# Optimization experiments

Measured on AMD Instinct MI355X. Metric: run time of the kernel, lower is better.

Reference implementation:

```python
import jax, jax.numpy as jnp
import numpy as np

B, IN, HID, OUT = 65536, 128, 256, 8


def setup_inputs() -> dict:
    key = jax.random.key(0)
    ks = jax.random.split(key, 9)
    def lin(kw, fan_in, fan_out):
        # torch nn.Linear default init: U(-1/sqrt(fan_in), 1/sqrt(fan_in))
        bound = 1.0 / np.sqrt(fan_in)
        kw1, kw2 = jax.random.split(kw)
        W = jax.random.uniform(kw1, (fan_out, fan_in), jnp.float32, -bound, bound)
        b = jax.random.uniform(kw2, (fan_out,), jnp.float32, -bound, bound)
        return W, b
    W1, b1 = lin(ks[0], 2 * IN, HID)
    W2, b2 = lin(ks[1], 2 * IN, HID)
    W3, b3 = lin(ks[2], HID + 3 * IN, HID)
    W4, b4 = lin(ks[3], HID, OUT)
    state = jax.random.normal(ks[4], (B, 3, IN), jnp.float32)
    return {"state": state, "W1": W1, "b1": b1, "W2": W2, "b2": b2,
            "W3": W3, "b3": b3, "W4": W4, "b4": b4}


def reference(state, W1, b1, W2, b2, W3, b3, W4, b4):
    # local_inputs = first 3 agents (state already [B,3,IN])
    local = state[:, :3]                              # [B,3,IN]
    agent = jnp.broadcast_to(local[:, :1], (local.shape[0], 2, local.shape[2]))
    neighbors = local[:, 1:3]                          # [B,2,IN]
    agents = jnp.concatenate([agent, neighbors], axis=-1)  # [B,2,2*IN]
    h_ij = jax.nn.relu(jnp.einsum('bnd,hd->bnh', agents, W1) + b1)  # [B,2,HID]
    e_ij = jax.nn.relu(jnp.einsum('bnd,hd->bnh', agents, W2) + b2)  # [B,2,HID]
    a_ij = jax.nn.softmax(e_ij, axis=1)                # softmax over neighbor dim
    h_i = jnp.sum(a_ij * h_ij, axis=1)                 # [B,HID]
    xxx = jnp.concatenate([h_i, local.reshape(local.shape[0], -1)], axis=-1)
    xxx = jax.nn.relu(xxx @ W3.T + b3)                 # [B,HID]
    return jnp.tanh(xxx @ W4.T + b4)                   # [B,OUT]
```

## Files before the change

### kernel.cpp

```cpp
#include <hip/hip_runtime.h>

typedef __bf16 bf16x8 __attribute__((ext_vector_type(8)));
typedef float  f32x4  __attribute__((ext_vector_type(4)));

__device__ __forceinline__ unsigned short f2bf(float f) {
  unsigned int u = __builtin_bit_cast(unsigned int, f);
  u = u + 0x7fffu + ((u >> 16) & 1u);
  return (unsigned short)(u >> 16);
}

#define O_W2 65536
#define O_W3 131072
#define O_W4 294912
#define N_PREP 299008

__global__ void prep_kernel(const float* __restrict__ W1, const float* __restrict__ W2,
                            const float* __restrict__ W3, const float* __restrict__ W4,
                            unsigned short* __restrict__ ws) {
  int id = blockIdx.x * 256 + threadIdx.x;
  if (id < O_W2) {
    ws[id] = f2bf(W1[id]);
  } else if (id < O_W3) {
    ws[id] = f2bf(W2[id - O_W2]);
  } else if (id < O_W4) {
    ws[id] = f2bf(W3[id - O_W3]);
  } else if (id < N_PREP) {
    int t = id - O_W4;
    ws[id] = (t < 2048) ? f2bf(W4[t]) : (unsigned short)0;
  }
}

#define XSTR 648
#define YSTR 264

__global__ __launch_bounds__(512, 2) void actor_kernel(
    const float* __restrict__ state,
    const float* __restrict__ b1, const float* __restrict__ b2,
    const float* __restrict__ b3, const float* __restrict__ b4,
    const unsigned short* __restrict__ wsb,
    float* __restrict__ out)
{
  __shared__ unsigned short xxx[64 * XSTR];
  __shared__ unsigned short ytl[64 * YSTR];

  const int tid  = threadIdx.x;
  const int w    = tid >> 6;
  const int lane = tid & 63;
  const int lr   = lane & 15;
  const int lg   = lane >> 4;
  const long b0  = (long)blockIdx.x * 64;

  {
    const float4* sp = (const float4*)(state + b0 * 384);
    #pragma unroll
    for (int t = 0; t < 12; ++t) {
      int f = tid + t * 512;
      float4 v = sp[f];
      int r   = f / 96;
      int rem = f - r * 96;
      int i   = rem >> 5;
      int k4  = (rem & 31) << 2;
      ushort4 u;
      u.x = f2bf(v.x); u.y = f2bf(v.y); u.z = f2bf(v.z); u.w = f2bf(v.w);
      *(ushort4*)&xxx[r * XSTR + 256 + i * 128 + k4] = u;
    }
  }
  __syncthreads();

  const int n0 = w * 32;

  #pragma unroll
  for (int sc = 0; sc < 2; ++sc) {
    const int ncol = n0 + sc * 16 + lr;
    f32x4 accH[8], accE[8];
    #pragma unroll
    for (int rt = 0; rt < 8; ++rt) {
      accH[rt] = (f32x4){0.f, 0.f, 0.f, 0.f};
      accE[rt] = (f32x4){0.f, 0.f, 0.f, 0.f};
    }
    const unsigned short* w1p = wsb + ncol * 256 + lg * 8;
    const unsigned short* w2p = wsb + O_W2 + ncol * 256 + lg * 8;

    bf16x8 bh = *(const bf16x8*)(w1p);
    bf16x8 be = *(const bf16x8*)(w2p);
    #pragma unroll
    for (int ks = 0; ks < 8; ++ks) {
      bf16x8 bhn, ben;
      if (ks < 7) {
        bhn = *(const bf16x8*)(w1p + (ks + 1) * 32);
        ben = *(const bf16x8*)(w2p + (ks + 1) * 32);
      }
      const int colo = (ks < 4) ? (256 + ks * 32 + lg * 8)
                                : (384 + (ks - 4) * 32 + lg * 8);
      #pragma unroll
      for (int rt = 0; rt < 8; ++rt) {
        const int m = rt * 16 + lr;
        const int addr = (m >> 1) * XSTR + colo + ((ks >= 4) ? ((m & 1) << 7) : 0);
        bf16x8 a = *(const bf16x8*)&xxx[addr];
        accH[rt] = __builtin_amdgcn_mfma_f32_16x16x32_bf16(a, bh, accH[rt], 0, 0, 0);
        accE[rt] = __builtin_amdgcn_mfma_f32_16x16x32_bf16(a, be, accE[rt], 0, 0, 0);
      }
      bh = bhn; be = ben;
    }

    const float b1v = b1[ncol];
    const float b2v = b2[ncol];
    #pragma unroll
    for (int rt = 0; rt < 8; ++rt) {
      const int r0 = rt * 8 + lg * 2;
      #pragma unroll
      for (int pr = 0; pr < 2; ++pr) {
        float h0 = fmaxf(accH[rt][2 * pr + 0] + b1v, 0.f);
        float h1 = fmaxf(accH[rt][2 * pr + 1] + b1v, 0.f);
        float e0 = fmaxf(accE[rt][2 * pr + 0] + b2v, 0.f);
        float e1 = fmaxf(accE[rt][2 * pr + 1] + b2v, 0.f);
        float a0 = 1.0f / (1.0f + __expf(e1 - e0));
        float hi = h1 + a0 * (h0 - h1);
        xxx[(r0 + pr) * XSTR + ncol] = f2bf(hi);
      }
    }
  }
  __syncthreads();

  {
    f32x4 acc3[4][2];
    #pragma unroll
    for (int rt = 0; rt < 4; ++rt) {
      acc3[rt][0] = (f32x4){0.f, 0.f, 0.f, 0.f};
      acc3[rt][1] = (f32x4){0.f, 0.f, 0.f, 0.f};
    }
    const unsigned short* w3pa = wsb + O_W3 + (n0 + lr) * 640 + lg * 8;
    const unsigned short* w3pb = wsb + O_W3 + (n0 + 16 + lr) * 640 + lg * 8;
    bf16x8 ba = *(const bf16x8*)(w3pa);
    bf16x8 bb = *(const bf16x8*)(w3pb);
    for (int ks = 0; ks < 20; ++ks) {
      bf16x8 ban, bbn;
      if (ks < 19) {
        ban = *(const bf16x8*)(w3pa + (ks + 1) * 32);
        bbn = *(const bf16x8*)(w3pb + (ks + 1) * 32);
      }
      #pragma unroll
      for (int rt = 0; rt < 4; ++rt) {
        bf16x8 a = *(const bf16x8*)&xxx[(rt * 16 + lr) * XSTR + ks * 32 + lg * 8];
        acc3[rt][0] = __builtin_amdgcn_mfma_f32_16x16x32_bf16(a, ba, acc3[rt][0], 0, 0, 0);
        acc3[rt][1] = __builtin_amdgcn_mfma_f32_16x16x32_bf16(a, bb, acc3[rt][1], 0, 0, 0);
      }
      ba = ban; bb = bbn;
    }
    const float b3a = b3[n0 + lr];
    const float b3b = b3[n0 + 16 + lr];
    #pragma unroll
    for (int rt = 0; rt < 4; ++rt) {
      #pragma unroll
      for (int reg = 0; reg < 4; ++reg) {
        int row = rt * 16 + lg * 4 + reg;
        float va = fmaxf(acc3[rt][0][reg] + b3a, 0.f);
        float vb = fmaxf(acc3[rt][1][reg] + b3b, 0.f);
        ytl[row * YSTR + n0 + lr]      = f2bf(va);
        ytl[row * YSTR + n0 + 16 + lr] = f2bf(vb);
      }
    }
  }
  __syncthreads();

  if (w < 4) {
    f32x4 acc4 = (f32x4){0.f, 0.f, 0.f, 0.f};
    const unsigned short* w4p = wsb + O_W4 + lr * 256 + lg * 8;
    #pragma unroll
    for (int ks = 0; ks < 8; ++ks) {
      bf16x8 a = *(const bf16x8*)&ytl[(w * 16 + lr) * YSTR + ks * 32 + lg * 8];
      bf16x8 b = *(const bf16x8*)(w4p + ks * 32);
      acc4 = __builtin_amdgcn_mfma_f32_16x16x32_bf16(a, b, acc4, 0, 0, 0);
    }
    if (lr < 8) {
      const float b4v = b4[lr];
      #pragma unroll
      for (int reg = 0; reg < 4; ++reg) {
        long row = b0 + w * 16 + lg * 4 + reg;
        out[row * 8 + lr] = tanhf(acc4[reg] + b4v);
      }
    }
  }
}

extern "C" void kernel_launch(void* const* d_in, const int* in_sizes, int n_in,
                              void* d_out, int out_size, void* d_ws, size_t ws_size,
                              hipStream_t stream) {
  const float* state = (const float*)d_in[0];
  const float* W1 = (const float*)d_in[1];
  const float* b1 = (const float*)d_in[2];
  const float* W2 = (const float*)d_in[3];
  const float* b2 = (const float*)d_in[4];
  const float* W3 = (const float*)d_in[5];
  const float* b3 = (const float*)d_in[6];
  const float* W4 = (const float*)d_in[7];
  const float* b4 = (const float*)d_in[8];

  unsigned short* wsb = (unsigned short*)d_ws;

  prep_kernel<<<(N_PREP + 255) / 256, 256, 0, stream>>>(W1, W2, W3, W4, wsb);
  actor_kernel<<<1024, 512, 0, stream>>>(state, b1, b2, b3, b4, wsb, (float*)d_out);
}
```

Before: 241.6 us.

## Split layer-1 GEMM by agent, persist blocks over 4 tiles with double-buffered state prefetch

```diff
diff --git a/kernel.cpp b/kernel.cpp
--- a/kernel.cpp
+++ b/kernel.cpp
@@ -30,8 +30,9 @@
   }
 }
 
-#define XSTR 648
-#define YSTR 264
+#define SB(r, c) ((r) * 384 + ((c) ^ (((r) & 7) << 3)))
+#define SH(r, c) ((r) * 256 + ((c) ^ (((r) & 7) << 3)))
+#define MFMA __builtin_amdgcn_mfma_f32_16x16x32_bf16
 
 __global__ __launch_bounds__(512, 2) void actor_kernel(
     const float* __restrict__ state,
@@ -40,146 +41,185 @@
     const unsigned short* __restrict__ wsb,
     float* __restrict__ out)
 {
-  __shared__ unsigned short xxx[64 * XSTR];
-  __shared__ unsigned short ytl[64 * YSTR];
+  __shared__ __align__(16) unsigned short sbuf[2][64 * 384];
+  __shared__ __align__(16) unsigned short hy[64 * 256];
 
   const int tid  = threadIdx.x;
   const int w    = tid >> 6;
   const int lane = tid & 63;
   const int lr   = lane & 15;
   const int lg   = lane >> 4;
-  const long b0  = (long)blockIdx.x * 64;
+  const long blk = blockIdx.x;
 
   {
-    const float4* sp = (const float4*)(state + b0 * 384);
+    const float4* sp = (const float4*)(state + blk * 256 * 384);
     #pragma unroll
-    for (int t = 0; t < 12; ++t) {
-      int f = tid + t * 512;
+    for (int i = 0; i < 12; ++i) {
+      int f = tid + i * 512;
       float4 v = sp[f];
-      int r   = f / 96;
-      int rem = f - r * 96;
-      int i   = rem >> 5;
-      int k4  = (rem & 31) << 2;
+      int r = f / 96, rem = f - r * 96;
       ushort4 u;
       u.x = f2bf(v.x); u.y = f2bf(v.y); u.z = f2bf(v.z); u.w = f2bf(v.w);
-      *(ushort4*)&xxx[r * XSTR + 256 + i * 128 + k4] = u;
+      *(ushort4*)&sbuf[0][SB(r, rem * 4)] = u;
     }
   }
   __syncthreads();
 
-  const int n0 = w * 32;
-
-  #pragma unroll
-  for (int sc = 0; sc < 2; ++sc) {
-    const int ncol = n0 + sc * 16 + lr;
-    f32x4 accH[8], accE[8];
-    #pragma unroll
-    for (int rt = 0; rt < 8; ++rt) {
-      accH[rt] = (f32x4){0.f, 0.f, 0.f, 0.f};
-      accE[rt] = (f32x4){0.f, 0.f, 0.f, 0.f};
-    }
-    const unsigned short* w1p = wsb + ncol * 256 + lg * 8;
-    const unsigned short* w2p = wsb + O_W2 + ncol * 256 + lg * 8;
-
-    bf16x8 bh = *(const bf16x8*)(w1p);
-    bf16x8 be = *(const bf16x8*)(w2p);
-    #pragma unroll
-    for (int ks = 0; ks < 8; ++ks) {
-      bf16x8 bhn, ben;
-      if (ks < 7) {
-        bhn = *(const bf16x8*)(w1p + (ks + 1) * 32);
-        ben = *(const bf16x8*)(w2p + (ks + 1) * 32);
-      }
-      const int colo = (ks < 4) ? (256 + ks * 32 + lg * 8)
-                                : (384 + (ks - 4) * 32 + lg * 8);
-      #pragma unroll
-      for (int rt = 0; rt < 8; ++rt) {
-        const int m = rt * 16 + lr;
-        const int addr = (m >> 1) * XSTR + colo + ((ks >= 4) ? ((m & 1) << 7) : 0);
-        bf16x8 a = *(const bf16x8*)&xxx[addr];
-        accH[rt] = __builtin_amdgcn_mfma_f32_16x16x32_bf16(a, bh, accH[rt], 0, 0, 0);
-        accE[rt] = __builtin_amdgcn_mfma_f32_16x16x32_bf16(a, be, accE[rt], 0, 0, 0);
-      }
-      bh = bhn; be = ben;
-    }
-
-    const float b1v = b1[ncol];
-    const float b2v = b2[ncol];
-    #pragma unroll
-    for (int rt = 0; rt < 8; ++rt) {
-      const int r0 = rt * 8 + lg * 2;
-      #pragma unroll
-      for (int pr = 0; pr < 2; ++pr) {
-        float h0 = fmaxf(accH[rt][2 * pr + 0] + b1v, 0.f);
-        float h1 = fmaxf(accH[rt][2 * pr + 1] + b1v, 0.f);
-        float e0 = fmaxf(accE[rt][2 * pr + 0] + b2v, 0.f);
-        float e1 = fmaxf(accE[rt][2 * pr + 1] + b2v, 0.f);
-        float a0 = 1.0f / (1.0f + __expf(e1 - e0));
-        float hi = h1 + a0 * (h0 - h1);
-        xxx[(r0 + pr) * XSTR + ncol] = f2bf(hi);
-      }
-    }
-  }
-  __syncthreads();
-
-  {
-    f32x4 acc3[4][2];
-    #pragma unroll
-    for (int rt = 0; rt < 4; ++rt) {
-      acc3[rt][0] = (f32x4){0.f, 0.f, 0.f, 0.f};
-      acc3[rt][1] = (f32x4){0.f, 0.f, 0.f, 0.f};
-    }
-    const unsigned short* w3pa = wsb + O_W3 + (n0 + lr) * 640 + lg * 8;
-    const unsigned short* w3pb = wsb + O_W3 + (n0 + 16 + lr) * 640 + lg * 8;
-    bf16x8 ba = *(const bf16x8*)(w3pa);
-    bf16x8 bb = *(const bf16x8*)(w3pb);
-    for (int ks = 0; ks < 20; ++ks) {
-      bf16x8 ban, bbn;
-      if (ks < 19) {
-        ban = *(const bf16x8*)(w3pa + (ks + 1) * 32);
-        bbn = *(const bf16x8*)(w3pb + (ks + 1) * 32);
-      }
-      #pragma unroll
-      for (int rt = 0; rt < 4; ++rt) {
-        bf16x8 a = *(const bf16x8*)&xxx[(rt * 16 + lr) * XSTR + ks * 32 + lg * 8];
-        acc3[rt][0] = __builtin_amdgcn_mfma_f32_16x16x32_bf16(a, ba, acc3[rt][0], 0, 0, 0);
-        acc3[rt][1] = __builtin_amdgcn_mfma_f32_16x16x32_bf16(a, bb, acc3[rt][1], 0, 0, 0);
-      }
-      ba = ban; bb = bbn;
-    }
-    const float b3a = b3[n0 + lr];
-    const float b3b = b3[n0 + 16 + lr];
-    #pragma unroll
-    for (int rt = 0; rt < 4; ++rt) {
-      #pragma unroll
-      for (int reg = 0; reg < 4; ++reg) {
-        int row = rt * 16 + lg * 4 + reg;
-        float va = fmaxf(acc3[rt][0][reg] + b3a, 0.f);
-        float vb = fmaxf(acc3[rt][1][reg] + b3b, 0.f);
-        ytl[row * YSTR + n0 + lr]      = f2bf(va);
-        ytl[row * YSTR + n0 + 16 + lr] = f2bf(vb);
-      }
-    }
-  }
-  __syncthreads();
-
-  if (w < 4) {
-    f32x4 acc4 = (f32x4){0.f, 0.f, 0.f, 0.f};
-    const unsigned short* w4p = wsb + O_W4 + lr * 256 + lg * 8;
-    #pragma unroll
-    for (int ks = 0; ks < 8; ++ks) {
-      bf16x8 a = *(const bf16x8*)&ytl[(w * 16 + lr) * YSTR + ks * 32 + lg * 8];
-      bf16x8 b = *(const bf16x8*)(w4p + ks * 32);
-      acc4 = __builtin_amdgcn_mfma_f32_16x16x32_bf16(a, b, acc4, 0, 0, 0);
-    }
-    if (lr < 8) {
-      const float b4v = b4[lr];
-      #pragma unroll
-      for (int reg = 0; reg < 4; ++reg) {
-        long row = b0 + w * 16 + lg * 4 + reg;
-        out[row * 8 + lr] = tanhf(acc4[reg] + b4v);
-      }
-    }
+  for (int t = 0; t < 4; ++t) {
+    const int cur = t & 1, nxt = cur ^ 1;
+    float4 sv[12];
+
+    #pragma unroll 2
+    for (int sc = 0; sc < 2; ++sc) {
+      const int nH = (w * 2 + sc) * 16;
+      bf16x8 wa1[4], wa2[4], wb1[4], wb2[4];
+      const unsigned short* p1 = wsb + (nH + lr) * 256 + lg * 8;
+      const unsigned short* p2 = wsb + O_W2 + (nH + lr) * 256 + lg * 8;
+      #pragma unroll
+      for (int kk = 0; kk < 4; ++kk) {
+        wa1[kk] = *(const bf16x8*)(p1 + kk * 32);
+        wa2[kk] = *(const bf16x8*)(p2 + kk * 32);
+        wb1[kk] = *(const bf16x8*)(p1 + 128 + kk * 32);
+        wb2[kk] = *(const bf16x8*)(p2 + 128 + kk * 32);
+      }
+      const float bv1 = b1[nH + lr];
+      const float bv2 = b2[nH + lr];
+
+      f32x4 aUh[4], aUe[4], aV1h[4], aV1e[4], aV2h[4], aV2e[4];
+      #pragma unroll
+      for (int rt = 0; rt < 4; ++rt) {
+        aUh[rt] = (f32x4){0.f,0.f,0.f,0.f};  aUe[rt] = (f32x4){0.f,0.f,0.f,0.f};
+        aV1h[rt] = (f32x4){0.f,0.f,0.f,0.f}; aV1e[rt] = (f32x4){0.f,0.f,0.f,0.f};
+        aV2h[rt] = (f32x4){0.f,0.f,0.f,0.f}; aV2e[rt] = (f32x4){0.f,0.f,0.f,0.f};
+      }
+
+      #pragma unroll
+      for (int kk = 0; kk < 4; ++kk) {
+        #pragma unroll
+        for (int rt = 0; rt < 4; ++rt) {
+          const int row = rt * 16 + lr;
+          bf16x8 a0 = *(const bf16x8*)&sbuf[cur][SB(row, kk * 32 + lg * 8)];
+          aUh[rt] = MFMA(a0, wa1[kk], aUh[rt], 0, 0, 0);
+          aUe[rt] = MFMA(a0, wa2[kk], aUe[rt], 0, 0, 0);
+          bf16x8 a1 = *(const bf16x8*)&sbuf[cur][SB(row, 128 + kk * 32 + lg * 8)];
+          aV1h[rt] = MFMA(a1, wb1[kk], aV1h[rt], 0, 0, 0);
+          aV1e[rt] = MFMA(a1, wb2[kk], aV1e[rt], 0, 0, 0);
+          bf16x8 a2 = *(const bf16x8*)&sbuf[cur][SB(row, 256 + kk * 32 + lg * 8)];
+          aV2h[rt] = MFMA(a2, wb1[kk], aV2h[rt], 0, 0, 0);
+          aV2e[rt] = MFMA(a2, wb2[kk], aV2e[rt], 0, 0, 0);
+        }
+      }
+
+      if (sc == 1 && t < 3) {
+        const float4* sp = (const float4*)(state + (blk * 256 + (t + 1) * 64) * 384);
+        #pragma unroll
+        for (int i = 0; i < 12; ++i) sv[i] = sp[tid + i * 512];
+      }
+
+      #pragma unroll
+      for (int rt = 0; rt < 4; ++rt) {
+        #pragma unroll
+        for (int reg = 0; reg < 4; ++reg) {
+          const int r = rt * 16 + lg * 4 + reg;
+          float uh = aUh[rt][reg], ue = aUe[rt][reg];
+          float h0 = fmaxf(uh + aV1h[rt][reg] + bv1, 0.f);
+          float h1 = fmaxf(uh + aV2h[rt][reg] + bv1, 0.f);
+          float e0 = fmaxf(ue + aV1e[rt][reg] + bv2, 0.f);
+          float e1 = fmaxf(ue + aV2e[rt][reg] + bv2, 0.f);
+          float a0w = 1.0f / (1.0f + __expf(e1 - e0));
+          hy[SH(r, nH + lr)] = f2bf(h1 + a0w * (h0 - h1));
+        }
+      }
+    }
+    __syncthreads();
+
+    if (t < 3) {
+      #pragma unroll
+      for (int i = 0; i < 12; ++i) {
+        int f = tid + i * 512;
+        int r = f / 96, rem = f - r * 96;
+        ushort4 u;
+        u.x = f2bf(sv[i].x); u.y = f2bf(sv[i].y); u.z = f2bf(sv[i].z); u.w = f2bf(sv[i].w);
+        *(ushort4*)&sbuf[nxt][SB(r, rem * 4)] = u;
+      }
+    }
+
+    {
+      const int n3 = w * 32;
+      const unsigned short* w3p = wsb + O_W3 + (n3 + lr) * 640 + lg * 8;
+      const float bv3a = b3[n3 + lr];
+      const float bv3b = b3[n3 + 16 + lr];
+      bf16x8 ring[4][2];
+      #pragma unroll
+      for (int k = 0; k < 3; ++k) {
+        ring[k][0] = *(const bf16x8*)(w3p + k * 32);
+        ring[k][1] = *(const bf16x8*)(w3p + 16 * 640 + k * 32);
+      }
+      f32x4 acc3[4][2];
+      #pragma unroll
+      for (int rt = 0; rt < 4; ++rt) {
+        acc3[rt][0] = (f32x4){0.f,0.f,0.f,0.f};
+        acc3[rt][1] = (f32x4){0.f,0.f,0.f,0.f};
+      }
+      #pragma unroll 4
+      for (int ks = 0; ks < 8; ++ks) {
+        ring[(ks + 3) & 3][0] = *(const bf16x8*)(w3p + (ks + 3) * 32);
+        ring[(ks + 3) & 3][1] = *(const bf16x8*)(w3p + 16 * 640 + (ks + 3) * 32);
+        #pragma unroll
+        for (int rt = 0; rt < 4; ++rt) {
+          bf16x8 a = *(const bf16x8*)&hy[SH(rt * 16 + lr, ks * 32 + lg * 8)];
+          acc3[rt][0] = MFMA(a, ring[ks & 3][0], acc3[rt][0], 0, 0, 0);
+          acc3[rt][1] = MFMA(a, ring[ks & 3][1], acc3[rt][1], 0, 0, 0);
+        }
+      }
+      #pragma unroll 4
+      for (int ks = 8; ks < 20; ++ks) {
+        if (ks < 17) {
+          ring[(ks + 3) & 3][0] = *(const bf16x8*)(w3p + (ks + 3) * 32);
+          ring[(ks + 3) & 3][1] = *(const bf16x8*)(w3p + 16 * 640 + (ks + 3) * 32);
+        }
+        #pragma unroll
+        for (int rt = 0; rt < 4; ++rt) {
+          bf16x8 a = *(const bf16x8*)&sbuf[cur][SB(rt * 16 + lr, (ks - 8) * 32 + lg * 8)];
+          acc3[rt][0] = MFMA(a, ring[ks & 3][0], acc3[rt][0], 0, 0, 0);
+          acc3[rt][1] = MFMA(a, ring[ks & 3][1], acc3[rt][1], 0, 0, 0);
+        }
+      }
+      __syncthreads();
+      #pragma unroll
+      for (int rt = 0; rt < 4; ++rt) {
+        #pragma unroll
+        for (int reg = 0; reg < 4; ++reg) {
+          const int row = rt * 16 + lg * 4 + reg;
+          hy[SH(row, n3 + lr)]      = f2bf(fmaxf(acc3[rt][0][reg] + bv3a, 0.f));
+          hy[SH(row, n3 + 16 + lr)] = f2bf(fmaxf(acc3[rt][1][reg] + bv3b, 0.f));
+        }
+      }
+    }
+    __syncthreads();
+
+    if (w < 4) {
+      f32x4 acc4 = (f32x4){0.f,0.f,0.f,0.f};
+      const unsigned short* w4p = wsb + O_W4 + lr * 256 + lg * 8;
+      #pragma unroll
+      for (int ks = 0; ks < 8; ++ks) {
+        bf16x8 a = *(const bf16x8*)&hy[SH(w * 16 + lr, ks * 32 + lg * 8)];
+        bf16x8 b = *(const bf16x8*)(w4p + ks * 32);
+        acc4 = MFMA(a, b, acc4, 0, 0, 0);
+      }
+      if (lr < 8) {
+        const float b4v = b4[lr];
+        #pragma unroll
+        for (int reg = 0; reg < 4; ++reg) {
+          float x = acc4[reg] + b4v;
+          float z = __expf(-2.f * fabsf(x));
+          float tv = (1.f - z) / (1.f + z);
+          long row = blk * 256 + t * 64 + w * 16 + lg * 4 + reg;
+          out[row * 8 + lr] = copysignf(tv, x);
+        }
+      }
+    }
+    __syncthreads();
   }
 }
 
@@ -199,5 +239,5 @@
   unsigned short* wsb = (unsigned short*)d_ws;
 
   prep_kernel<<<(N_PREP + 255) / 256, 256, 0, stream>>>(W1, W2, W3, W4, wsb);
-  actor_kernel<<<1024, 512, 0, stream>>>(state, b1, b2, b3, b4, wsb, (float*)d_out);
-}
+  actor_kernel<<<256, 512, 0, stream>>>(state, b1, b2, b3, b4, wsb, (float*)d_out);
+}
```

After: 335.5 us. 1.39x slower.
